# Optimization experiments

Hardware: AMD Instinct MI355X
Metric: run time of the kernel (lower is better)

Reference implementation:

```python
import jax, jax.numpy as jnp
import numpy as np

B, N, E, D, R, O, L = 256, 128, 2048, 512, 1024, 10, 5


def setup_inputs() -> dict:
    key = jax.random.key(0)
    k0, k1, k2, k3, k4 = jax.random.split(key, 5)
    x = jax.random.normal(k0, (B, N, D), jnp.float32)
    edges = jax.random.randint(k1, (B, 2, E), 0, N)  # per-graph COO (src,dst)
    xav = (6.0 / (D + 1 + R)) ** 0.5  # xavier_uniform for cp-pool W
    W_cp = jax.random.uniform(k2, (L, D + 1, R), jnp.float32, -xav, xav)
    lin_w = jax.random.normal(k3, (L, R, O), jnp.float32) * 0.03
    lin_b = jax.random.normal(k4, (L, O), jnp.float32) * 0.01
    return {"x": x, "edges": edges, "W_cp": W_cp, "lin_w": lin_w, "lin_b": lin_b}


def _cp_pool(h, W):
    # graph_cp_pooling: append ones column, tanh(x @ W), prod over nodes
    ones = jnp.ones(h.shape[:-1] + (1,), h.dtype)
    hn = jnp.concatenate([h, ones], axis=-1)  # [B, N, D+1]
    fea = jnp.tanh(jnp.einsum('bnd,dr->bnr', hn, W))  # [B, N, R]
    return jnp.prod(fea, axis=1)  # [B, R]


def _aggregate(h, src, dst):
    # pooled = (I + A) @ h  with sum neighbor pooling (learn_eps=False)
    gathered = jnp.take_along_axis(h, src[..., None], axis=1)  # [B, E, D]
    b_idx = jnp.arange(h.shape[0])[:, None]  # [B, 1]
    agg = jnp.zeros_like(h).at[b_idx, dst].add(gathered)  # scatter-add to dst
    return h + agg


def reference(x, edges, W_cp, lin_w, lin_b):
    src, dst = edges[:, 0], edges[:, 1]
    h = x
    # layer 0 readout on raw features (dropout is identity in eval mode)
    score = _cp_pool(h, W_cp[0]) @ lin_w[0] + lin_b[0]
    for layer in range(1, L):
        h = _aggregate(h, src, dst)
        score = score + _cp_pool(h, W_cp[layer]) @ lin_w[layer] + lin_b[layer]
    return score  # [B, O]
```

## Files before the change

kernel.cpp:

```cpp
#include <hip/hip_runtime.h>
#include <math.h>

#define B 256
#define N 128
#define E 2048
#define D 512
#define R 1024
#define O 10
#define L 5
#define BK 32

typedef unsigned short u16;
typedef unsigned int u32;
typedef __bf16 bf16x8 __attribute__((ext_vector_type(8)));
typedef u16 u16x8 __attribute__((ext_vector_type(8)));
typedef float floatx4 __attribute__((ext_vector_type(4)));

__device__ inline u16 f2bf(float f) {
    union { float f; u32 u; } v; v.f = f;
    u32 u = v.u;
    return (u16)((u + 0x7fffu + ((u >> 16) & 1u)) >> 16);
}
__device__ inline float bf2f(u16 s) {
    union { u32 u; float f; } v; v.u = ((u32)s) << 16;
    return v.f;
}

__device__ inline float fast_tanh(float x) {
    return 1.0f - 2.0f / (__expf(2.0f * x) + 1.0f);
}

__device__ inline void gload16(const void* g, void* l) {
    __builtin_amdgcn_global_load_lds(
        (const __attribute__((address_space(1))) void*)g,
        (__attribute__((address_space(3))) void*)l, 16, 0, 0);
}

__device__ inline bf16x8 ldsfrag(const u16* p) {
    u16x8 v = *(const u16x8*)p;
    return __builtin_bit_cast(bf16x8, v);
}

__global__ void zero_kernel(float* __restrict__ p, size_t n) {
    size_t i = (size_t)blockIdx.x * blockDim.x + threadIdx.x;
    size_t stride = (size_t)gridDim.x * blockDim.x;
    for (; i < n; i += stride) p[i] = 0.f;
}

__global__ void fill_adj_kernel(const int* __restrict__ edges, float* __restrict__ C) {
    int idx = blockIdx.x * blockDim.x + threadIdx.x;
    if (idx >= B * E) return;
    int b = idx / E;
    int e = idx - b * E;
    int src = edges[b * 2 * E + e];
    int dst = edges[b * 2 * E + E + e];
    atomicAdd(&C[(size_t)b * N * N + (size_t)dst * N + src], 1.0f);
}

__global__ void diag_kernel(float* __restrict__ C) {
    int idx = blockIdx.x * blockDim.x + threadIdx.x;
    if (idx >= B * N) return;
    C[(size_t)(idx >> 7) * N * N + (size_t)(idx & 127) * 129] += 1.0f;
}

__global__ void cbf_kernel(const float4* __restrict__ C4, ushort4* __restrict__ o, size_t n4) {
    size_t i = (size_t)blockIdx.x * blockDim.x + threadIdx.x;
    size_t stride = (size_t)gridDim.x * blockDim.x;
    for (; i < n4; i += stride) {
        float4 v = C4[i];
        ushort4 r;
        r.x = f2bf(v.x); r.y = f2bf(v.y); r.z = f2bf(v.z); r.w = f2bf(v.w);
        o[i] = r;
    }
}

__global__ void split_kernel(const float4* __restrict__ x4,
                             uint2* __restrict__ hi4, uint2* __restrict__ lo4, size_t n4) {
    size_t i = (size_t)blockIdx.x * blockDim.x + threadIdx.x;
    size_t stride = (size_t)gridDim.x * blockDim.x;
    for (; i < n4; i += stride) {
        float4 v = x4[i];
        u16 h0 = f2bf(v.x), h1 = f2bf(v.y), h2 = f2bf(v.z), h3 = f2bf(v.w);
        uint2 hp; hp.x = (u32)h0 | ((u32)h1 << 16); hp.y = (u32)h2 | ((u32)h3 << 16);
        hi4[i] = hp;
        u16 l0 = f2bf(v.x - bf2f(h0)), l1 = f2bf(v.y - bf2f(h1));
        u16 l2 = f2bf(v.z - bf2f(h2)), l3 = f2bf(v.w - bf2f(h3));
        uint2 lp; lp.x = (u32)l0 | ((u32)l1 << 16); lp.y = (u32)l2 | ((u32)l3 << 16);
        lo4[i] = lp;
    }
}

__global__ __launch_bounds__(256)
void wt_split_kernel(const float* __restrict__ W_cp,
                     u16* __restrict__ Wt_hi, u16* __restrict__ Wt_lo) {
    __shared__ float t[64][65];
    const int l = blockIdx.z, k0 = blockIdx.y * 64, r0 = blockIdx.x * 64;
    const float* Wl = W_cp + (size_t)l * 513 * 1024;
    const int tx = threadIdx.x & 63, ty = threadIdx.x >> 6;
#pragma unroll
    for (int p = 0; p < 16; ++p) {
        int k = ty + p * 4;
        t[k][tx] = Wl[(size_t)(k0 + k) * 1024 + r0 + tx];
    }
    __syncthreads();
    u16* oh = Wt_hi + ((size_t)l * 1024 + r0) * 512 + k0;
    u16* ol = Wt_lo + ((size_t)l * 1024 + r0) * 512 + k0;
#pragma unroll
    for (int p = 0; p < 16; ++p) {
        int r = ty + p * 4;
        float v = t[tx][r];
        u16 hv = f2bf(v);
        oh[(size_t)r * 512 + tx] = hv;
        ol[(size_t)r * 512 + tx] = f2bf(v - bf2f(hv));
    }
}

__global__ __launch_bounds__(256)
void cp_pool_mfma_kernel(const u16* __restrict__ h_hi, const u16* __restrict__ h_lo,
                         const u16* __restrict__ Wt_hi, const u16* __restrict__ Wt_lo,
                         const float* __restrict__ Wbias,
                         float* __restrict__ prod_out)
{
    __shared__ u16 As_hi[128 * BK], As_lo[128 * BK];
    __shared__ u16 Bs_hi[128 * BK], Bs_lo[128 * BK];
    __shared__ float red[2][128];

    const int flat = blockIdx.x;
    const int s    = flat >> 3;
    const int b    = (flat & 7) * 32 + (s >> 3);
    const int r0   = (s & 7) * 128;

    const int tid = threadIdx.x;
    const int w    = tid >> 6;
    const int lane = tid & 63;
    const int rb = w & 1;
    const int cb = w >> 1;

    floatx4 acc[4][4];
#pragma unroll
    for (int i = 0; i < 4; ++i)
#pragma unroll
        for (int j = 0; j < 4; ++j)
#pragma unroll
            for (int k = 0; k < 4; ++k) acc[i][j][k] = 0.f;

    const int srow = w * 32 + (lane >> 2);
    const int kswz = (((lane & 3) ^ ((lane >> 3) & 3)) * 8);
    const u16* gAh = h_hi + ((size_t)b * 128 + srow) * 512 + kswz;
    const u16* gAl = h_lo + ((size_t)b * 128 + srow) * 512 + kswz;
    const u16* gBh = Wt_hi + (size_t)(r0 + srow) * 512 + kswz;
    const u16* gBl = Wt_lo + (size_t)(r0 + srow) * 512 + kswz;

    const int am = rb * 64 + (lane & 15);
    const int bn = cb * 64 + (lane & 15);
    const int ko = (((lane >> 4) ^ ((lane >> 1) & 3)) * 8);

#pragma unroll
    for (int it = 0; it < 2; ++it) {
        const size_t go = (size_t)it * 16 * 512;
        const int ld = (w * 2 + it) * 512;
        gload16(gAh + go, As_hi + ld);
        gload16(gAl + go, As_lo + ld);
        gload16(gBh + go, Bs_hi + ld);
        gload16(gBl + go, Bs_lo + ld);
    }
    gAh += BK; gAl += BK; gBh += BK; gBl += BK;

    for (int ks = 0; ks < 16; ++ks) {
        __syncthreads();

        bf16x8 ah[4], al[4], bh[4], bl[4];
#pragma unroll
        for (int t = 0; t < 4; ++t) {
            ah[t] = ldsfrag(&As_hi[(am + t * 16) * BK + ko]);
            al[t] = ldsfrag(&As_lo[(am + t * 16) * BK + ko]);
            bh[t] = ldsfrag(&Bs_hi[(bn + t * 16) * BK + ko]);
            bl[t] = ldsfrag(&Bs_lo[(bn + t * 16) * BK + ko]);
        }
        __syncthreads();

        if (ks < 15) {
#pragma unroll
            for (int it = 0; it < 2; ++it) {
                const size_t go = (size_t)it * 16 * 512;
                const int ld = (w * 2 + it) * 512;
                gload16(gAh + go, As_hi + ld);
                gload16(gAl + go, As_lo + ld);
                gload16(gBh + go, Bs_hi + ld);
                gload16(gBl + go, Bs_lo + ld);
            }
            gAh += BK; gAl += BK; gBh += BK; gBl += BK;
        }

#pragma unroll
        for (int i = 0; i < 4; ++i)
#pragma unroll
            for (int j = 0; j < 4; ++j) {
                acc[i][j] = __builtin_amdgcn_mfma_f32_16x16x32_bf16(al[i], bh[j], acc[i][j], 0, 0, 0);
                acc[i][j] = __builtin_amdgcn_mfma_f32_16x16x32_bf16(ah[i], bl[j], acc[i][j], 0, 0, 0);
                acc[i][j] = __builtin_amdgcn_mfma_f32_16x16x32_bf16(ah[i], bh[j], acc[i][j], 0, 0, 0);
            }
    }

    const int quad = lane >> 4;
    const int c16  = lane & 15;
#pragma unroll
    for (int tj = 0; tj < 4; ++tj) {
        const int c = cb * 64 + tj * 16 + c16;
        const float bias = Wbias[r0 + c];
        float p = 1.f;
#pragma unroll
        for (int ti = 0; ti < 4; ++ti)
#pragma unroll
            for (int ri = 0; ri < 4; ++ri)
                p *= fast_tanh(acc[ti][tj][ri] + bias);
        p *= __shfl_xor(p, 16, 64);
        p *= __shfl_xor(p, 32, 64);
        if (quad == 0) red[rb][c] = p;
    }
    __syncthreads();
    if (tid < 128)
        prod_out[(size_t)b * R + r0 + tid] = red[0][tid] * red[1][tid];
}

__global__ __launch_bounds__(256)
void aggregate_mfma_kernel(const u16* __restrict__ hi_in, const u16* __restrict__ lo_in,
                           const u16* __restrict__ Cbf,
                           u16* __restrict__ hi_out, u16* __restrict__ lo_out)
{
    __shared__ u16 Cs[128 * 32];
    __shared__ u16 Bs_hi[128 * 40];
    __shared__ u16 Bs_lo[128 * 40];

    const int flat = blockIdx.x;
    const int rest = flat >> 3;
    const int b    = (flat & 7) * 32 + (rest >> 2);
    const int d0   = (rest & 3) * 128;

    const int tid  = threadIdx.x;
    const int w    = tid >> 6;
    const int lane = tid & 63;
    const int rb   = w & 1;
    const int cb   = w >> 1;

    floatx4 acc[4][4];
#pragma unroll
    for (int i = 0; i < 4; ++i)
#pragma unroll
        for (int j = 0; j < 4; ++j)
#pragma unroll
            for (int k = 0; k < 4; ++k) acc[i][j][k] = 0.f;

    const int kswz = (((lane & 3) ^ ((lane >> 3) & 3)) * 8);
    const u16* gC = Cbf + ((size_t)b * 128 + (w * 32 + (lane >> 2))) * 128 + kswz;

    const int ssi = tid >> 3;
    const int dg  = (tid & 7) * 16;
    const u16* gBh = hi_in + ((size_t)b * 128 + ssi) * 512 + d0 + dg;
    const u16* gBl = lo_in + ((size_t)b * 128 + ssi) * 512 + d0 + dg;

    const int am  = rb * 64 + (lane & 15);
    const int ko  = (((lane >> 4) ^ ((lane >> 1) & 3)) * 8);
    const int bko = (lane >> 4) * 8;

    for (int s0 = 0; s0 < 128; s0 += 32) {
#pragma unroll
        for (int it = 0; it < 2; ++it)
            gload16(gC + s0 + (size_t)it * 16 * 128, Cs + (w * 2 + it) * 512);

        {
            const u16* ph = gBh + (size_t)s0 * 512;
            const u16* pl = gBl + (size_t)s0 * 512;
            uint4 a0 = *(const uint4*)ph;
            uint4 a1 = *(const uint4*)(ph + 8);
            uint4 b0 = *(const uint4*)pl;
            uint4 b1 = *(const uint4*)(pl + 8);
            const u16* av0 = (const u16*)&a0; const u16* av1 = (const u16*)&a1;
            const u16* bv0 = (const u16*)&b0; const u16* bv1 = (const u16*)&b1;
#pragma unroll
            for (int i = 0; i < 8; ++i) {
                Bs_hi[(dg + i) * 40 + ssi]     = av0[i];
                Bs_hi[(dg + 8 + i) * 40 + ssi] = av1[i];
                Bs_lo[(dg + i) * 40 + ssi]     = bv0[i];
                Bs_lo[(dg + 8 + i) * 40 + ssi] = bv1[i];
            }
        }
        __syncthreads();

        bf16x8 af[4], bhf[4], blf[4];
#pragma unroll
        for (int t = 0; t < 4; ++t) {
            af[t]  = ldsfrag(&Cs[(am + t * 16) * 32 + ko]);
            const int d = cb * 64 + t * 16 + (lane & 15);
            bhf[t] = ldsfrag(&Bs_hi[d * 40 + bko]);
            blf[t] = ldsfrag(&Bs_lo[d * 40 + bko]);
        }
#pragma unroll
        for (int i = 0; i < 4; ++i)
#pragma unroll
            for (int j = 0; j < 4; ++j) {
                acc[i][j] = __builtin_amdgcn_mfma_f32_16x16x32_bf16(af[i], bhf[j], acc[i][j], 0, 0, 0);
                acc[i][j] = __builtin_amdgcn_mfma_f32_16x16x32_bf16(af[i], blf[j], acc[i][j], 0, 0, 0);
            }
        __syncthreads();
    }

    const int quad = lane >> 4;
    const int c16  = lane & 15;
#pragma unroll
    for (int i = 0; i < 4; ++i)
#pragma unroll
        for (int j = 0; j < 4; ++j) {
            const int d = d0 + cb * 64 + j * 16 + c16;
#pragma unroll
            for (int ri = 0; ri < 4; ++ri) {
                const int n = rb * 64 + i * 16 + quad * 4 + ri;
                size_t o = ((size_t)b * 128 + n) * 512 + d;
                float v = acc[i][j][ri];
                u16 hv = f2bf(v);
                hi_out[o] = hv;
                lo_out[o] = f2bf(v - bf2f(hv));
            }
        }
}

__global__ __launch_bounds__(256)
void score_kernel(const float* __restrict__ prod,
                  const float* __restrict__ lin_w,
                  const float* __restrict__ lin_b,
                  float* __restrict__ out)
{
    const int b   = blockIdx.x;
    const int tid = threadIdx.x;

    float acc[O];
#pragma unroll
    for (int o = 0; o < O; ++o) acc[o] = 0.f;

    for (int l = 0; l < L; ++l) {
        const float* pl = prod + ((size_t)l * B + b) * R;
        const float* wl = lin_w + (size_t)l * R * O;
        for (int r = tid; r < R; r += 256) {
            const float p = pl[r];
#pragma unroll
            for (int o = 0; o < O; ++o)
                acc[o] = fmaf(p, wl[r * O + o], acc[o]);
        }
    }

    __shared__ float sb[256];
    for (int o = 0; o < O; ++o) {
        sb[tid] = acc[o];
        __syncthreads();
        for (int off = 128; off > 0; off >>= 1) {
            if (tid < off) sb[tid] += sb[tid + off];
            __syncthreads();
        }
        if (tid == 0) {
            float bias = 0.f;
            for (int l = 0; l < L; ++l) bias += lin_b[l * O + o];
            out[b * O + o] = sb[0] + bias;
        }
        __syncthreads();
    }
}

extern "C" void kernel_launch(void* const* d_in, const int* in_sizes, int n_in,
                              void* d_out, int out_size, void* d_ws, size_t ws_size,
                              hipStream_t stream) {
    const float* x     = (const float*)d_in[0];
    const int*   edges = (const int*)d_in[1];
    const float* W_cp  = (const float*)d_in[2];
    const float* lin_w = (const float*)d_in[3];
    const float* lin_b = (const float*)d_in[4];
    float*       out   = (float*)d_out;

    char* ws = (char*)d_ws;
    const size_t C_BYTES   = (size_t)B * N * N * 4;
    const size_t CBF_BYTES = (size_t)B * N * N * 2;
    const size_t HH_BYTES  = (size_t)B * N * D * 2;
    const size_t WT_BYTES  = (size_t)L * 1024 * 512 * 2;

    float* C     = (float*)ws;                    ws += C_BYTES;
    u16*   Cbf   = (u16*)ws;                      ws += CBF_BYTES;
    u16*   hiA   = (u16*)ws;                      ws += HH_BYTES;
    u16*   loA   = (u16*)ws;                      ws += HH_BYTES;
    u16*   hiB   = (u16*)ws;                      ws += HH_BYTES;
    u16*   loB   = (u16*)ws;                      ws += HH_BYTES;
    u16*   Wt_hi = (u16*)ws;                      ws += WT_BYTES;
    u16*   Wt_lo = (u16*)ws;                      ws += WT_BYTES;
    float* prod  = (float*)ws;

    zero_kernel<<<1024, 256, 0, stream>>>(C, (size_t)B * N * N);
    fill_adj_kernel<<<(B * E + 255) / 256, 256, 0, stream>>>(edges, C);
    diag_kernel<<<(B * N + 255) / 256, 256, 0, stream>>>(C);
    cbf_kernel<<<1024, 256, 0, stream>>>((const float4*)C, (ushort4*)Cbf,
                                         (size_t)B * N * N / 4);
    wt_split_kernel<<<dim3(16, 8, L), 256, 0, stream>>>(W_cp, Wt_hi, Wt_lo);
    split_kernel<<<2048, 256, 0, stream>>>((const float4*)x, (uint2*)hiA, (uint2*)loA,
                                           (size_t)B * N * D / 4);

    cp_pool_mfma_kernel<<<2048, 256, 0, stream>>>(
        hiA, loA, Wt_hi, Wt_lo, W_cp + (size_t)512 * 1024, prod);

    const u16* phi = hiA; const u16* plo = loA;
    u16* bhi[2] = {hiB, hiA};
    u16* blo[2] = {loB, loA};
    for (int l = 1; l < L; ++l) {
        u16* nhi = bhi[(l - 1) & 1];
        u16* nlo = blo[(l - 1) & 1];
        aggregate_mfma_kernel<<<1024, 256, 0, stream>>>(phi, plo, Cbf, nhi, nlo);
        cp_pool_mfma_kernel<<<2048, 256, 0, stream>>>(
            nhi, nlo,
            Wt_hi + (size_t)l * 1024 * 512, Wt_lo + (size_t)l * 1024 * 512,
            W_cp + ((size_t)l * 513 + 512) * 1024,
            prod + (size_t)l * B * R);
        phi = nhi; plo = nlo;
    }

    score_kernel<<<B, 256, 0, stream>>>(prod, lin_w, lin_b, out);
}
```

Baseline: 813.9 us.

## Store hidden states in MFMA fragment-packed layout and load A operands from global into registers

Hidden-state hi/lo bf16 buffers are written in a layout pre-packed to match the MFMA 16x16x32 operand fragment order. The split and aggregate kernels now emit this layout, and the aggregate kernel reads from it. The cp_pool kernel then drops its A-side shared-memory staging and loads A fragments straight from global memory into registers, double-buffered one k-step ahead. This removes LDS traffic and shared memory for A, which could improve occupancy, at the cost of more register pressure and scattered per-element stores in the aggregate epilogue.

```diff
diff --git a/kernel.cpp b/kernel.cpp
--- a/kernel.cpp
+++ b/kernel.cpp
@@ -16,6 +16,7 @@
 typedef u16 u16x8 __attribute__((ext_vector_type(8)));
 typedef float floatx4 __attribute__((ext_vector_type(4)));
 
+
 __device__ inline u16 f2bf(float f) {
     union { float f; u32 u; } v; v.f = f;
     u32 u = v.u;
@@ -38,6 +39,10 @@
 
 __device__ inline bf16x8 ldsfrag(const u16* p) {
     u16x8 v = *(const u16x8*)p;
+    return __builtin_bit_cast(bf16x8, v);
+}
+__device__ inline bf16x8 gfrag(const u16* p) {
+    uint4 v = *(const uint4*)p;
     return __builtin_bit_cast(bf16x8, v);
 }
 
@@ -75,18 +80,23 @@
 }
 
 __global__ void split_kernel(const float4* __restrict__ x4,
-                             uint2* __restrict__ hi4, uint2* __restrict__ lo4, size_t n4) {
+                             u16* __restrict__ hp_hi, u16* __restrict__ hp_lo, size_t n4) {
     size_t i = (size_t)blockIdx.x * blockDim.x + threadIdx.x;
     size_t stride = (size_t)gridDim.x * blockDim.x;
     for (; i < n4; i += stride) {
         float4 v = x4[i];
+        const int d0 = ((int)(i & 127)) * 4;
+        const int n  = (int)((i >> 7) & 127);
+        const int bb = (int)(i >> 14);
         u16 h0 = f2bf(v.x), h1 = f2bf(v.y), h2 = f2bf(v.z), h3 = f2bf(v.w);
         uint2 hp; hp.x = (u32)h0 | ((u32)h1 << 16); hp.y = (u32)h2 | ((u32)h3 << 16);
-        hi4[i] = hp;
         u16 l0 = f2bf(v.x - bf2f(h0)), l1 = f2bf(v.y - bf2f(h1));
         u16 l2 = f2bf(v.z - bf2f(h2)), l3 = f2bf(v.w - bf2f(h3));
         uint2 lp; lp.x = (u32)l0 | ((u32)l1 << 16); lp.y = (u32)l2 | ((u32)l3 << 16);
-        lo4[i] = lp;
+        const int lane_p = (n & 15) + 16 * ((d0 >> 3) & 3);
+        size_t e = ((((size_t)bb * 8 + (n >> 4)) * 16 + (d0 >> 5)) * 64 + lane_p) * 8 + (d0 & 7);
+        *(uint2*)(hp_hi + e) = hp;
+        *(uint2*)(hp_lo + e) = lp;
     }
 }
 
@@ -116,12 +126,11 @@
 }
 
 __global__ __launch_bounds__(256)
-void cp_pool_mfma_kernel(const u16* __restrict__ h_hi, const u16* __restrict__ h_lo,
+void cp_pool_mfma_kernel(const u16* __restrict__ hp_hi, const u16* __restrict__ hp_lo,
                          const u16* __restrict__ Wt_hi, const u16* __restrict__ Wt_lo,
                          const float* __restrict__ Wbias,
                          float* __restrict__ prod_out)
 {
-    __shared__ u16 As_hi[128 * BK], As_lo[128 * BK];
     __shared__ u16 Bs_hi[128 * BK], Bs_lo[128 * BK];
     __shared__ float red[2][128];
 
@@ -130,11 +139,11 @@
     const int b    = (flat & 7) * 32 + (s >> 3);
     const int r0   = (s & 7) * 128;
 
-    const int tid = threadIdx.x;
+    const int tid  = threadIdx.x;
     const int w    = tid >> 6;
     const int lane = tid & 63;
-    const int rb = w & 1;
-    const int cb = w >> 1;
+    const int rb   = w & 1;
+    const int cb   = w >> 1;
 
     floatx4 acc[4][4];
 #pragma unroll
@@ -146,61 +155,61 @@
 
     const int srow = w * 32 + (lane >> 2);
     const int kswz = (((lane & 3) ^ ((lane >> 3) & 3)) * 8);
-    const u16* gAh = h_hi + ((size_t)b * 128 + srow) * 512 + kswz;
-    const u16* gAl = h_lo + ((size_t)b * 128 + srow) * 512 + kswz;
     const u16* gBh = Wt_hi + (size_t)(r0 + srow) * 512 + kswz;
     const u16* gBl = Wt_lo + (size_t)(r0 + srow) * 512 + kswz;
 
-    const int am = rb * 64 + (lane & 15);
+    const size_t baseA = (size_t)(b * 8 + rb * 4) * 8192 + lane * 8;
+
     const int bn = cb * 64 + (lane & 15);
     const int ko = (((lane >> 4) ^ ((lane >> 1) & 3)) * 8);
 
+    bf16x8 a_hi[2][4], a_lo[2][4];
+
 #pragma unroll
     for (int it = 0; it < 2; ++it) {
-        const size_t go = (size_t)it * 16 * 512;
-        const int ld = (w * 2 + it) * 512;
-        gload16(gAh + go, As_hi + ld);
-        gload16(gAl + go, As_lo + ld);
-        gload16(gBh + go, Bs_hi + ld);
-        gload16(gBl + go, Bs_lo + ld);
-    }
-    gAh += BK; gAl += BK; gBh += BK; gBl += BK;
-
-    for (int ks = 0; ks < 16; ++ks) {
-        __syncthreads();
-
-        bf16x8 ah[4], al[4], bh[4], bl[4];
+        gload16(gBh + (size_t)it * 16 * 512, Bs_hi + (w * 2 + it) * 512);
+        gload16(gBl + (size_t)it * 16 * 512, Bs_lo + (w * 2 + it) * 512);
+    }
+    gBh += BK; gBl += BK;
+#pragma unroll
+    for (int t = 0; t < 4; ++t) {
+        a_hi[0][t] = gfrag(hp_hi + baseA + t * 8192);
+        a_lo[0][t] = gfrag(hp_lo + baseA + t * 8192);
+    }
+
+    auto step = [&](int ks, int p) {
+        __syncthreads();
+        bf16x8 bh[4], bl[4];
 #pragma unroll
         for (int t = 0; t < 4; ++t) {
-            ah[t] = ldsfrag(&As_hi[(am + t * 16) * BK + ko]);
-            al[t] = ldsfrag(&As_lo[(am + t * 16) * BK + ko]);
             bh[t] = ldsfrag(&Bs_hi[(bn + t * 16) * BK + ko]);
             bl[t] = ldsfrag(&Bs_lo[(bn + t * 16) * BK + ko]);
         }
         __syncthreads();
-
         if (ks < 15) {
 #pragma unroll
             for (int it = 0; it < 2; ++it) {
-                const size_t go = (size_t)it * 16 * 512;
-                const int ld = (w * 2 + it) * 512;
-                gload16(gAh + go, As_hi + ld);
-                gload16(gAl + go, As_lo + ld);
-                gload16(gBh + go, Bs_hi + ld);
-                gload16(gBl + go, Bs_lo + ld);
-            }
-            gAh += BK; gAl += BK; gBh += BK; gBl += BK;
-        }
-
+                gload16(gBh + (size_t)it * 16 * 512, Bs_hi + (w * 2 + it) * 512);
+                gload16(gBl + (size_t)it * 16 * 512, Bs_lo + (w * 2 + it) * 512);
+            }
+            gBh += BK; gBl += BK;
+            const size_t off = baseA + (size_t)(ks + 1) * 512;
+#pragma unroll
+            for (int t = 0; t < 4; ++t) {
+                a_hi[1 - p][t] = gfrag(hp_hi + off + t * 8192);
+                a_lo[1 - p][t] = gfrag(hp_lo + off + t * 8192);
+            }
+        }
 #pragma unroll
         for (int i = 0; i < 4; ++i)
 #pragma unroll
             for (int j = 0; j < 4; ++j) {
-                acc[i][j] = __builtin_amdgcn_mfma_f32_16x16x32_bf16(al[i], bh[j], acc[i][j], 0, 0, 0);
-                acc[i][j] = __builtin_amdgcn_mfma_f32_16x16x32_bf16(ah[i], bl[j], acc[i][j], 0, 0, 0);
-                acc[i][j] = __builtin_amdgcn_mfma_f32_16x16x32_bf16(ah[i], bh[j], acc[i][j], 0, 0, 0);
-            }
-    }
+                acc[i][j] = __builtin_amdgcn_mfma_f32_16x16x32_bf16(a_lo[p][i], bh[j], acc[i][j], 0, 0, 0);
+                acc[i][j] = __builtin_amdgcn_mfma_f32_16x16x32_bf16(a_hi[p][i], bl[j], acc[i][j], 0, 0, 0);
+                acc[i][j] = __builtin_amdgcn_mfma_f32_16x16x32_bf16(a_hi[p][i], bh[j], acc[i][j], 0, 0, 0);
+            }
+    };
+    for (int ks = 0; ks < 16; ks += 2) { step(ks, 0); step(ks + 1, 1); }
 
     const int quad = lane >> 4;
     const int c16  = lane & 15;
@@ -224,9 +233,9 @@
 }
 
 __global__ __launch_bounds__(256)
-void aggregate_mfma_kernel(const u16* __restrict__ hi_in, const u16* __restrict__ lo_in,
+void aggregate_mfma_kernel(const u16* __restrict__ hp_hi, const u16* __restrict__ hp_lo,
                            const u16* __restrict__ Cbf,
-                           u16* __restrict__ hi_out, u16* __restrict__ lo_out)
+                           u16* __restrict__ ho_hi, u16* __restrict__ ho_lo)
 {
     __shared__ u16 Cs[128 * 32];
     __shared__ u16 Bs_hi[128 * 40];
@@ -256,8 +265,7 @@
 
     const int ssi = tid >> 3;
     const int dg  = (tid & 7) * 16;
-    const u16* gBh = hi_in + ((size_t)b * 128 + ssi) * 512 + d0 + dg;
-    const u16* gBl = lo_in + ((size_t)b * 128 + ssi) * 512 + d0 + dg;
+    const int dA  = d0 + dg;
 
     const int am  = rb * 64 + (lane & 15);
     const int ko  = (((lane >> 4) ^ ((lane >> 1) & 3)) * 8);
@@ -269,12 +277,13 @@
             gload16(gC + s0 + (size_t)it * 16 * 128, Cs + (w * 2 + it) * 512);
 
         {
-            const u16* ph = gBh + (size_t)s0 * 512;
-            const u16* pl = gBl + (size_t)s0 * 512;
-            uint4 a0 = *(const uint4*)ph;
-            uint4 a1 = *(const uint4*)(ph + 8);
-            uint4 b0 = *(const uint4*)pl;
-            uint4 b1 = *(const uint4*)(pl + 8);
+            const int sg = s0 + ssi;
+            size_t e0 = ((((size_t)b * 8 + (sg >> 4)) * 16 + (dA >> 5)) * 64
+                         + ((sg & 15) + 16 * ((dA >> 3) & 3))) * 8;
+            uint4 a0 = *(const uint4*)(hp_hi + e0);
+            uint4 a1 = *(const uint4*)(hp_hi + e0 + 128);
+            uint4 b0 = *(const uint4*)(hp_lo + e0);
+            uint4 b1 = *(const uint4*)(hp_lo + e0 + 128);
             const u16* av0 = (const u16*)&a0; const u16* av1 = (const u16*)&a1;
             const u16* bv0 = (const u16*)&b0; const u16* bv1 = (const u16*)&b1;
 #pragma unroll
@@ -311,15 +320,20 @@
     for (int i = 0; i < 4; ++i)
 #pragma unroll
         for (int j = 0; j < 4; ++j) {
-            const int d = d0 + cb * 64 + j * 16 + c16;
+            const int D0 = d0 + cb * 64 + j * 16;
+            const int kc = D0 >> 5;
+            const int lp_base = 16 * (((D0 >> 3) + (c16 >> 3)) & 3);
+            const int jp = c16 & 7;
+            const int n16 = rb * 4 + i;
+            const size_t fb = (((size_t)b * 8 + n16) * 16 + kc) * 64;
 #pragma unroll
             for (int ri = 0; ri < 4; ++ri) {
-                const int n = rb * 64 + i * 16 + quad * 4 + ri;
-                size_t o = ((size_t)b * 128 + n) * 512 + d;
+                const int nlow = quad * 4 + ri;
+                size_t o = (fb + nlow + lp_base) * 8 + jp;
                 float v = acc[i][j][ri];
                 u16 hv = f2bf(v);
-                hi_out[o] = hv;
-                lo_out[o] = f2bf(v - bf2f(hv));
+                ho_hi[o] = hv;
+                ho_lo[o] = f2bf(v - bf2f(hv));
             }
         }
 }
@@ -397,7 +411,7 @@
     cbf_kernel<<<1024, 256, 0, stream>>>((const float4*)C, (ushort4*)Cbf,
                                          (size_t)B * N * N / 4);
     wt_split_kernel<<<dim3(16, 8, L), 256, 0, stream>>>(W_cp, Wt_hi, Wt_lo);
-    split_kernel<<<2048, 256, 0, stream>>>((const float4*)x, (uint2*)hiA, (uint2*)loA,
+    split_kernel<<<2048, 256, 0, stream>>>((const float4*)x, hiA, loA,
                                            (size_t)B * N * D / 4);
 
     cp_pool_mfma_kernel<<<2048, 256, 0, stream>>>(
```

New measurement: 880.2 us. +8.2%, slower.

## Load MFMA fragments directly from global memory with pre-packed weight layout

Applied to the files above, without the earlier changes.

The cp-pool GEMM no longer stages A and B tiles through LDS with barriers. Each wave now loads its bf16 fragments straight from global memory into registers, double-buffered in software across k-steps. To make the weight loads coalesced, wt_split now writes W in a fragment-packed layout so each lane reads contiguous 16 bytes. This removes LDS traffic and the two barriers per k-step. In exchange it costs more VGPRs, and every wave re-reads A and B from L2 with no cross-wave sharing, which raises global and L2 load volume.

```diff
diff --git a/kernel.cpp b/kernel.cpp
--- a/kernel.cpp
+++ b/kernel.cpp
@@ -38,6 +38,10 @@
 
 __device__ inline bf16x8 ldsfrag(const u16* p) {
     u16x8 v = *(const u16x8*)p;
+    return __builtin_bit_cast(bf16x8, v);
+}
+__device__ inline bf16x8 gfrag(const u16* p) {
+    uint4 v = *(const uint4*)p;
     return __builtin_bit_cast(bf16x8, v);
 }
 
@@ -92,7 +96,7 @@
 
 __global__ __launch_bounds__(256)
 void wt_split_kernel(const float* __restrict__ W_cp,
-                     u16* __restrict__ Wt_hi, u16* __restrict__ Wt_lo) {
+                     u16* __restrict__ Wp_hi, u16* __restrict__ Wp_lo) {
     __shared__ float t[64][65];
     const int l = blockIdx.z, k0 = blockIdx.y * 64, r0 = blockIdx.x * 64;
     const float* Wl = W_cp + (size_t)l * 513 * 1024;
@@ -103,26 +107,35 @@
         t[k][tx] = Wl[(size_t)(k0 + k) * 1024 + r0 + tx];
     }
     __syncthreads();
-    u16* oh = Wt_hi + ((size_t)l * 1024 + r0) * 512 + k0;
-    u16* ol = Wt_lo + ((size_t)l * 1024 + r0) * 512 + k0;
-#pragma unroll
-    for (int p = 0; p < 16; ++p) {
-        int r = ty + p * 4;
-        float v = t[tx][r];
-        u16 hv = f2bf(v);
-        oh[(size_t)r * 512 + tx] = hv;
-        ol[(size_t)r * 512 + tx] = f2bf(v - bf2f(hv));
+#pragma unroll
+    for (int p = 0; p < 2; ++p) {
+        const int slot = threadIdx.x * 2 + p;
+        const int lane = slot & 63;
+        const int kst  = (slot >> 6) & 1;
+        const int r16t = slot >> 7;
+        const int rin  = r16t * 16 + (lane & 15);
+        const int kin  = kst * 32 + (lane >> 4) * 8;
+        u16 hv[8], lv[8];
+#pragma unroll
+        for (int j = 0; j < 8; ++j) {
+            float v = t[kin + j][rin];
+            hv[j] = f2bf(v);
+            lv[j] = f2bf(v - bf2f(hv[j]));
+        }
+        const int rg = (r0 >> 4) + r16t;
+        const int ks = (k0 >> 5) + kst;
+        size_t base = (((size_t)l * 64 + rg) * 16 + ks) * 512 + (size_t)lane * 8;
+        *(uint4*)(Wp_hi + base) = *(const uint4*)hv;
+        *(uint4*)(Wp_lo + base) = *(const uint4*)lv;
     }
 }
 
 __global__ __launch_bounds__(256)
 void cp_pool_mfma_kernel(const u16* __restrict__ h_hi, const u16* __restrict__ h_lo,
-                         const u16* __restrict__ Wt_hi, const u16* __restrict__ Wt_lo,
+                         const u16* __restrict__ Wp_hi, const u16* __restrict__ Wp_lo,
                          const float* __restrict__ Wbias,
                          float* __restrict__ prod_out)
 {
-    __shared__ u16 As_hi[128 * BK], As_lo[128 * BK];
-    __shared__ u16 Bs_hi[128 * BK], Bs_lo[128 * BK];
     __shared__ float red[2][128];
 
     const int flat = blockIdx.x;
@@ -130,11 +143,11 @@
     const int b    = (flat & 7) * 32 + (s >> 3);
     const int r0   = (s & 7) * 128;
 
-    const int tid = threadIdx.x;
+    const int tid  = threadIdx.x;
     const int w    = tid >> 6;
     const int lane = tid & 63;
-    const int rb = w & 1;
-    const int cb = w >> 1;
+    const int rb   = w & 1;
+    const int cb   = w >> 1;
 
     floatx4 acc[4][4];
 #pragma unroll
@@ -144,63 +157,50 @@
 #pragma unroll
             for (int k = 0; k < 4; ++k) acc[i][j][k] = 0.f;
 
-    const int srow = w * 32 + (lane >> 2);
-    const int kswz = (((lane & 3) ^ ((lane >> 3) & 3)) * 8);
-    const u16* gAh = h_hi + ((size_t)b * 128 + srow) * 512 + kswz;
-    const u16* gAl = h_lo + ((size_t)b * 128 + srow) * 512 + kswz;
-    const u16* gBh = Wt_hi + (size_t)(r0 + srow) * 512 + kswz;
-    const u16* gBl = Wt_lo + (size_t)(r0 + srow) * 512 + kswz;
-
-    const int am = rb * 64 + (lane & 15);
-    const int bn = cb * 64 + (lane & 15);
-    const int ko = (((lane >> 4) ^ ((lane >> 1) & 3)) * 8);
-
-#pragma unroll
-    for (int it = 0; it < 2; ++it) {
-        const size_t go = (size_t)it * 16 * 512;
-        const int ld = (w * 2 + it) * 512;
-        gload16(gAh + go, As_hi + ld);
-        gload16(gAl + go, As_lo + ld);
-        gload16(gBh + go, Bs_hi + ld);
-        gload16(gBl + go, Bs_lo + ld);
-    }
-    gAh += BK; gAl += BK; gBh += BK; gBl += BK;
-
-    for (int ks = 0; ks < 16; ++ks) {
-        __syncthreads();
-
-        bf16x8 ah[4], al[4], bh[4], bl[4];
-#pragma unroll
-        for (int t = 0; t < 4; ++t) {
-            ah[t] = ldsfrag(&As_hi[(am + t * 16) * BK + ko]);
-            al[t] = ldsfrag(&As_lo[(am + t * 16) * BK + ko]);
-            bh[t] = ldsfrag(&Bs_hi[(bn + t * 16) * BK + ko]);
-            bl[t] = ldsfrag(&Bs_lo[(bn + t * 16) * BK + ko]);
-        }
-        __syncthreads();
-
-        if (ks < 15) {
-#pragma unroll
-            for (int it = 0; it < 2; ++it) {
-                const size_t go = (size_t)it * 16 * 512;
-                const int ld = (w * 2 + it) * 512;
-                gload16(gAh + go, As_hi + ld);
-                gload16(gAl + go, As_lo + ld);
-                gload16(gBh + go, Bs_hi + ld);
-                gload16(gBl + go, Bs_lo + ld);
-            }
-            gAh += BK; gAl += BK; gBh += BK; gBl += BK;
-        }
-
-#pragma unroll
-        for (int i = 0; i < 4; ++i)
-#pragma unroll
-            for (int j = 0; j < 4; ++j) {
-                acc[i][j] = __builtin_amdgcn_mfma_f32_16x16x32_bf16(al[i], bh[j], acc[i][j], 0, 0, 0);
-                acc[i][j] = __builtin_amdgcn_mfma_f32_16x16x32_bf16(ah[i], bl[j], acc[i][j], 0, 0, 0);
-                acc[i][j] = __builtin_amdgcn_mfma_f32_16x16x32_bf16(ah[i], bh[j], acc[i][j], 0, 0, 0);
-            }
-    }
+    const size_t aOff = ((size_t)b * 128 + rb * 64 + (lane & 15)) * 512 + ((lane >> 4) * 8);
+    const size_t bOff = (((size_t)((s & 7) * 8 + cb * 4)) * 16) * 512 + (size_t)lane * 8;
+
+    bf16x8 Ah[2][4], Al[2][4], Bh[2][4], Bl[2][4];
+
+#define LOADSTEP(ks, p)                                                        \
+    {                                                                          \
+        _Pragma("unroll")                                                      \
+        for (int t = 0; t < 4; ++t) {                                          \
+            const size_t ao = aOff + (size_t)t * 8192 + (size_t)(ks) * 32;     \
+            Ah[p][t] = gfrag(h_hi + ao);                                       \
+            Al[p][t] = gfrag(h_lo + ao);                                       \
+            const size_t bo = bOff + (size_t)t * 8192 + (size_t)(ks) * 512;    \
+            Bh[p][t] = gfrag(Wp_hi + bo);                                      \
+            Bl[p][t] = gfrag(Wp_lo + bo);                                      \
+        }                                                                      \
+    }
+
+#define MFMASTEP(p)                                                            \
+    {                                                                          \
+        _Pragma("unroll")                                                      \
+        for (int i = 0; i < 4; ++i)                                            \
+            _Pragma("unroll")                                                  \
+            for (int j = 0; j < 4; ++j) {                                      \
+                acc[i][j] = __builtin_amdgcn_mfma_f32_16x16x32_bf16(           \
+                    Al[p][i], Bh[p][j], acc[i][j], 0, 0, 0);                   \
+                acc[i][j] = __builtin_amdgcn_mfma_f32_16x16x32_bf16(           \
+                    Ah[p][i], Bl[p][j], acc[i][j], 0, 0, 0);                   \
+                acc[i][j] = __builtin_amdgcn_mfma_f32_16x16x32_bf16(           \
+                    Ah[p][i], Bh[p][j], acc[i][j], 0, 0, 0);                   \
+            }                                                                  \
+    }
+
+    LOADSTEP(0, 0)
+    LOADSTEP(1, 1)
+#pragma unroll
+    for (int ks = 0; ks < 16; ks += 2) {
+        MFMASTEP(0)
+        if (ks + 2 < 16) LOADSTEP(ks + 2, 0)
+        MFMASTEP(1)
+        if (ks + 3 < 16) LOADSTEP(ks + 3, 1)
+    }
+#undef LOADSTEP
+#undef MFMASTEP
 
     const int quad = lane >> 4;
     const int c16  = lane & 15;
@@ -379,7 +379,7 @@
     const size_t C_BYTES   = (size_t)B * N * N * 4;
     const size_t CBF_BYTES = (size_t)B * N * N * 2;
     const size_t HH_BYTES  = (size_t)B * N * D * 2;
-    const size_t WT_BYTES  = (size_t)L * 1024 * 512 * 2;
+    const size_t WP_BYTES  = (size_t)L * 64 * 16 * 512 * 2;
 
     float* C     = (float*)ws;                    ws += C_BYTES;
     u16*   Cbf   = (u16*)ws;                      ws += CBF_BYTES;
@@ -387,8 +387,8 @@
     u16*   loA   = (u16*)ws;                      ws += HH_BYTES;
     u16*   hiB   = (u16*)ws;                      ws += HH_BYTES;
     u16*   loB   = (u16*)ws;                      ws += HH_BYTES;
-    u16*   Wt_hi = (u16*)ws;                      ws += WT_BYTES;
-    u16*   Wt_lo = (u16*)ws;                      ws += WT_BYTES;
+    u16*   Wp_hi = (u16*)ws;                      ws += WP_BYTES;
+    u16*   Wp_lo = (u16*)ws;                      ws += WP_BYTES;
     float* prod  = (float*)ws;
 
     zero_kernel<<<1024, 256, 0, stream>>>(C, (size_t)B * N * N);
@@ -396,12 +396,14 @@
     diag_kernel<<<(B * N + 255) / 256, 256, 0, stream>>>(C);
     cbf_kernel<<<1024, 256, 0, stream>>>((const float4*)C, (ushort4*)Cbf,
                                          (size_t)B * N * N / 4);
-    wt_split_kernel<<<dim3(16, 8, L), 256, 0, stream>>>(W_cp, Wt_hi, Wt_lo);
+    wt_split_kernel<<<dim3(16, 8, L), 256, 0, stream>>>(W_cp, Wp_hi, Wp_lo);
     split_kernel<<<2048, 256, 0, stream>>>((const float4*)x, (uint2*)hiA, (uint2*)loA,
                                            (size_t)B * N * D / 4);
 
+    const size_t WP_L = (size_t)64 * 16 * 512;
+
     cp_pool_mfma_kernel<<<2048, 256, 0, stream>>>(
-        hiA, loA, Wt_hi, Wt_lo, W_cp + (size_t)512 * 1024, prod);
+        hiA, loA, Wp_hi, Wp_lo, W_cp + (size_t)512 * 1024, prod);
 
     const u16* phi = hiA; const u16* plo = loA;
     u16* bhi[2] = {hiB, hiA};
@@ -412,7 +414,7 @@
         aggregate_mfma_kernel<<<1024, 256, 0, stream>>>(phi, plo, Cbf, nhi, nlo);
         cp_pool_mfma_kernel<<<2048, 256, 0, stream>>>(
             nhi, nlo,
-            Wt_hi + (size_t)l * 1024 * 512, Wt_lo + (size_t)l * 1024 * 512,
+            Wp_hi + (size_t)l * WP_L, Wp_lo + (size_t)l * WP_L,
             W_cp + ((size_t)l * 513 + 512) * 1024,
             prod + (size_t)l * B * R);
         phi = nhi; plo = nlo;
```

After: 1.063 ms. 30.6% more time.

## Enlarge cp-pool GEMM tile to 256x256 with 512-thread blocks

Applied to the files above, without the earlier changes.

Reworks the cp-pool MFMA kernel so each 512-thread block computes a 256-row (two graphs) by 256-column tile instead of 128x128, with each wave holding a 64x128 accumulator. Each loaded A and B fragment is reused across more MFMAs, which reduces global and LDS traffic per flop. The grid drops from 2048 to 512 blocks. The cost is higher register pressure (128 accumulator floats per thread plus 24 fragment registers) under launch_bounds(512,2), a risk of spills or lower occupancy, and fewer blocks to balance across CUs.

```diff
diff --git a/kernel.cpp b/kernel.cpp
--- a/kernel.cpp
+++ b/kernel.cpp
@@ -115,98 +115,96 @@
     }
 }
 
-__global__ __launch_bounds__(256)
+__global__ __launch_bounds__(512, 2)
 void cp_pool_mfma_kernel(const u16* __restrict__ h_hi, const u16* __restrict__ h_lo,
                          const u16* __restrict__ Wt_hi, const u16* __restrict__ Wt_lo,
                          const float* __restrict__ Wbias,
                          float* __restrict__ prod_out)
 {
-    __shared__ u16 As_hi[128 * BK], As_lo[128 * BK];
-    __shared__ u16 Bs_hi[128 * BK], Bs_lo[128 * BK];
-    __shared__ float red[2][128];
+    __shared__ u16 SS[4][256 * BK];
 
     const int flat = blockIdx.x;
-    const int s    = flat >> 3;
-    const int b    = (flat & 7) * 32 + (s >> 3);
-    const int r0   = (s & 7) * 128;
-
-    const int tid = threadIdx.x;
+    const int xcd  = flat & 7;
+    const int idx  = flat >> 3;
+    const int bp   = xcd * 16 + (idx >> 2);
+    const int r0   = (idx & 3) * 256;
+
+    const int tid  = threadIdx.x;
     const int w    = tid >> 6;
     const int lane = tid & 63;
-    const int rb = w & 1;
-    const int cb = w >> 1;
-
-    floatx4 acc[4][4];
+    const int rb   = w & 3;
+    const int cb   = w >> 2;
+
+    floatx4 acc[4][8];
 #pragma unroll
     for (int i = 0; i < 4; ++i)
 #pragma unroll
-        for (int j = 0; j < 4; ++j)
+        for (int j = 0; j < 8; ++j)
 #pragma unroll
             for (int k = 0; k < 4; ++k) acc[i][j][k] = 0.f;
 
-    const int srow = w * 32 + (lane >> 2);
-    const int kswz = (((lane & 3) ^ ((lane >> 3) & 3)) * 8);
-    const u16* gAh = h_hi + ((size_t)b * 128 + srow) * 512 + kswz;
-    const u16* gAl = h_lo + ((size_t)b * 128 + srow) * 512 + kswz;
-    const u16* gBh = Wt_hi + (size_t)(r0 + srow) * 512 + kswz;
-    const u16* gBl = Wt_lo + (size_t)(r0 + srow) * 512 + kswz;
+    const int lrow = lane >> 2;
+    const int g8   = (((lane & 3) ^ ((lane >> 3) & 3)) * 8);
+    const u16* gA_h = h_hi  + ((size_t)bp * 256 + w * 32 + lrow) * 512 + g8;
+    const u16* gA_l = h_lo  + ((size_t)bp * 256 + w * 32 + lrow) * 512 + g8;
+    const u16* gB_h = Wt_hi + ((size_t)(r0 + w * 32 + lrow)) * 512 + g8;
+    const u16* gB_l = Wt_lo + ((size_t)(r0 + w * 32 + lrow)) * 512 + g8;
+    const int ldst = w * 1024 + lane * 8;
 
     const int am = rb * 64 + (lane & 15);
-    const int bn = cb * 64 + (lane & 15);
+    const int bn = cb * 128 + (lane & 15);
     const int ko = (((lane >> 4) ^ ((lane >> 1) & 3)) * 8);
 
-#pragma unroll
-    for (int it = 0; it < 2; ++it) {
-        const size_t go = (size_t)it * 16 * 512;
-        const int ld = (w * 2 + it) * 512;
-        gload16(gAh + go, As_hi + ld);
-        gload16(gAl + go, As_lo + ld);
-        gload16(gBh + go, Bs_hi + ld);
-        gload16(gBl + go, Bs_lo + ld);
-    }
-    gAh += BK; gAl += BK; gBh += BK; gBl += BK;
+#define DMASTEP(ks)                                                            \
+    {                                                                          \
+        const size_t go = (size_t)(ks) * BK;                                   \
+        gload16(gA_h + go, &SS[0][ldst]);                                      \
+        gload16(gA_h + go + 16 * 512, &SS[0][ldst + 512]);                     \
+        gload16(gA_l + go, &SS[1][ldst]);                                      \
+        gload16(gA_l + go + 16 * 512, &SS[1][ldst + 512]);                     \
+        gload16(gB_h + go, &SS[2][ldst]);                                      \
+        gload16(gB_h + go + 16 * 512, &SS[2][ldst + 512]);                     \
+        gload16(gB_l + go, &SS[3][ldst]);                                      \
+        gload16(gB_l + go + 16 * 512, &SS[3][ldst + 512]);                     \
+    }
+
+    DMASTEP(0)
 
     for (int ks = 0; ks < 16; ++ks) {
         __syncthreads();
 
-        bf16x8 ah[4], al[4], bh[4], bl[4];
+        bf16x8 ah[4], al[4], bh[8], bl[8];
 #pragma unroll
         for (int t = 0; t < 4; ++t) {
-            ah[t] = ldsfrag(&As_hi[(am + t * 16) * BK + ko]);
-            al[t] = ldsfrag(&As_lo[(am + t * 16) * BK + ko]);
-            bh[t] = ldsfrag(&Bs_hi[(bn + t * 16) * BK + ko]);
-            bl[t] = ldsfrag(&Bs_lo[(bn + t * 16) * BK + ko]);
-        }
-        __syncthreads();
-
-        if (ks < 15) {
-#pragma unroll
-            for (int it = 0; it < 2; ++it) {
-                const size_t go = (size_t)it * 16 * 512;
-                const int ld = (w * 2 + it) * 512;
-                gload16(gAh + go, As_hi + ld);
-                gload16(gAl + go, As_lo + ld);
-                gload16(gBh + go, Bs_hi + ld);
-                gload16(gBl + go, Bs_lo + ld);
-            }
-            gAh += BK; gAl += BK; gBh += BK; gBl += BK;
-        }
+            ah[t] = ldsfrag(&SS[0][(am + t * 16) * BK + ko]);
+            al[t] = ldsfrag(&SS[1][(am + t * 16) * BK + ko]);
+        }
+#pragma unroll
+        for (int t = 0; t < 8; ++t) {
+            bh[t] = ldsfrag(&SS[2][(bn + t * 16) * BK + ko]);
+            bl[t] = ldsfrag(&SS[3][(bn + t * 16) * BK + ko]);
+        }
+        __syncthreads();
+
+        if (ks < 15) DMASTEP(ks + 1)
 
 #pragma unroll
         for (int i = 0; i < 4; ++i)
 #pragma unroll
-            for (int j = 0; j < 4; ++j) {
+            for (int j = 0; j < 8; ++j) {
                 acc[i][j] = __builtin_amdgcn_mfma_f32_16x16x32_bf16(al[i], bh[j], acc[i][j], 0, 0, 0);
                 acc[i][j] = __builtin_amdgcn_mfma_f32_16x16x32_bf16(ah[i], bl[j], acc[i][j], 0, 0, 0);
                 acc[i][j] = __builtin_amdgcn_mfma_f32_16x16x32_bf16(ah[i], bh[j], acc[i][j], 0, 0, 0);
             }
     }
-
+#undef DMASTEP
+
+    float* red = (float*)&SS[0][0];
     const int quad = lane >> 4;
     const int c16  = lane & 15;
 #pragma unroll
-    for (int tj = 0; tj < 4; ++tj) {
-        const int c = cb * 64 + tj * 16 + c16;
+    for (int tj = 0; tj < 8; ++tj) {
+        const int c = cb * 128 + tj * 16 + c16;
         const float bias = Wbias[r0 + c];
         float p = 1.f;
 #pragma unroll
@@ -216,11 +214,16 @@
                 p *= fast_tanh(acc[ti][tj][ri] + bias);
         p *= __shfl_xor(p, 16, 64);
         p *= __shfl_xor(p, 32, 64);
-        if (quad == 0) red[rb][c] = p;
+        if (quad == 0) red[rb * 256 + c] = p;
     }
     __syncthreads();
-    if (tid < 128)
-        prod_out[(size_t)b * R + r0 + tid] = red[0][tid] * red[1][tid];
+    {
+        const int t    = tid & 255;
+        const int half = tid >> 8;
+        const int b    = bp * 2 + half;
+        const float v  = red[(half * 2) * 256 + t] * red[(half * 2 + 1) * 256 + t];
+        prod_out[(size_t)b * R + r0 + t] = v;
+    }
 }
 
 __global__ __launch_bounds__(256)
@@ -400,7 +403,7 @@
     split_kernel<<<2048, 256, 0, stream>>>((const float4*)x, (uint2*)hiA, (uint2*)loA,
                                            (size_t)B * N * D / 4);
 
-    cp_pool_mfma_kernel<<<2048, 256, 0, stream>>>(
+    cp_pool_mfma_kernel<<<512, 512, 0, stream>>>(
         hiA, loA, Wt_hi, Wt_lo, W_cp + (size_t)512 * 1024, prod);
 
     const u16* phi = hiA; const u16* plo = loA;
@@ -410,7 +413,7 @@
         u16* nhi = bhi[(l - 1) & 1];
         u16* nlo = blo[(l - 1) & 1];
         aggregate_mfma_kernel<<<1024, 256, 0, stream>>>(phi, plo, Cbf, nhi, nlo);
-        cp_pool_mfma_kernel<<<2048, 256, 0, stream>>>(
+        cp_pool_mfma_kernel<<<512, 512, 0, stream>>>(
             nhi, nlo,
             Wt_hi + (size_t)l * 1024 * 512, Wt_lo + (size_t)l * 1024 * 512,
             W_cp + ((size_t)l * 513 + 512) * 1024,
```

Result: faster. 748.1 us (-8.1%).
